# Optimization experiments

Measured on AMD Instinct MI355X. Metric: run time of the kernel, lower is better.

The kernel has to match this reference:

```python
import jax, jax.numpy as jnp
import numpy as np

N_NODES = 100000
N_EDGES = 600000
D = 128
BN_EPS = 1e-5


def setup_inputs() -> dict:
    key = jax.random.key(0)
    k1, k2, k3 = jax.random.split(key, 3)
    x = jax.random.normal(k1, (N_NODES, D), dtype=jnp.float32)
    edge_index = jax.random.randint(k2, (2, N_EDGES), 0, N_NODES, dtype=jnp.int64)
    # Linear(in=D, out=D): kaiming-uniform-ish init
    W = jax.random.normal(k3, (D, D), dtype=jnp.float32) / np.sqrt(D)
    b = jnp.zeros((D,), dtype=jnp.float32)
    eps_gin = jnp.zeros((), dtype=jnp.float32)  # train_eps=True, init 0
    gamma = jnp.ones((D,), dtype=jnp.float32)
    beta = jnp.zeros((D,), dtype=jnp.float32)
    return {"x": x, "edge_index": edge_index, "W": W, "b": b,
            "eps_gin": eps_gin, "gamma": gamma, "beta": beta}


def reference(x, edge_index, W, b, eps_gin, gamma, beta):
    src, dst = edge_index[0], edge_index[1]
    # GIN aggregation: sum of source features into destination nodes
    agg = jax.ops.segment_sum(x[src], dst, num_segments=N_NODES)  # [N, D]
    h = (1.0 + eps_gin) * x + agg
    # MLP([D, D]) == single Linear (PyG plain_last)
    h = jnp.einsum('nd,df->nf', h, W.T) + b  # torch Linear: h @ W^T + b
    # BatchNorm1d in training mode (batch stats, biased variance)
    mean = jnp.mean(h, axis=0)
    var = jnp.mean((h - mean) ** 2, axis=0)
    h = (h - mean) * jax.lax.rsqrt(var + BN_EPS) * gamma + beta
    h = jax.nn.relu(h)
    # residual
    return h + x
```

## Files before the change

### kernel.cpp

```cpp
#include <hip/hip_runtime.h>
#include <hip/hip_bf16.h>
#include <hip/hip_cooperative_groups.h>

namespace cg = cooperative_groups;

#define N_NODES 100000
#define N_EDGES 600000
#define D 128
#define BN_EPS 1e-5f
#define CAP 32
#define CAST_BLOCKS 6250
#define FILL_BLOCKS ((N_EDGES + 255) / 256)

typedef __bf16 bf16x8 __attribute__((ext_vector_type(8)));
typedef float floatx4 __attribute__((ext_vector_type(4)));
typedef unsigned short ushortx8 __attribute__((ext_vector_type(8)));

__device__ __forceinline__ unsigned short f2bf(float f) {
    union { float f; unsigned u; } v; v.f = f;
    unsigned u = v.u;
    unsigned r = u + 0x7FFFu + ((u >> 16) & 1u);
    return (unsigned short)(r >> 16);
}
__device__ __forceinline__ float bf2f(unsigned short u) {
    union { unsigned u; float f; } v; v.u = ((unsigned)u) << 16;
    return v.f;
}

__global__ __launch_bounds__(256) void k_prep(const float* __restrict__ x,
                                              const int* __restrict__ ei,
                                              int* __restrict__ cursor,
                                              int* __restrict__ bucket,
                                              unsigned short* __restrict__ xb) {
    int b = blockIdx.x;
    if (b < CAST_BLOCKS) {
        int idx = (b * 256 + threadIdx.x) * 8;
        float4 a = *(const float4*)(x + idx);
        float4 c = *(const float4*)(x + idx + 4);
        ushortx8 u;
        u[0] = f2bf(a.x); u[1] = f2bf(a.y); u[2] = f2bf(a.z); u[3] = f2bf(a.w);
        u[4] = f2bf(c.x); u[5] = f2bf(c.y); u[6] = f2bf(c.z); u[7] = f2bf(c.w);
        *(ushortx8*)(xb + idx) = u;
    } else {
        int e = (b - CAST_BLOCKS) * 256 + threadIdx.x;
        if (e >= N_EDGES) return;
        int src = ei[e];
        int dst = ei[N_EDGES + e];
        int pos = atomicAdd(&cursor[dst], 1);
        if (pos < CAP) bucket[dst * CAP + pos] = src;
    }
}

__global__ __launch_bounds__(256) void k_aggregate(const unsigned short* __restrict__ xb,
                                                   const int* __restrict__ cursor,
                                                   const int* __restrict__ bucket,
                                                   const float* __restrict__ epsp,
                                                   unsigned short* __restrict__ h) {
    int tid = blockIdx.x * 256 + threadIdx.x;
    int node = tid >> 4;
    if (node >= N_NODES) return;
    int lane = tid & 15;
    int deg = cursor[node];
    if (deg > CAP) deg = CAP;
    const int* bk = bucket + node * CAP;
    float acc[8] = {0.f, 0.f, 0.f, 0.f, 0.f, 0.f, 0.f, 0.f};
    for (int i = 0; i < deg; ++i) {
        int s = bk[i];
        ushortx8 v = *(const ushortx8*)(xb + (size_t)s * D + lane * 8);
#pragma unroll
        for (int j = 0; j < 8; ++j) acc[j] += bf2f(v[j]);
    }
    const float one_eps = 1.0f + epsp[0];
    ushortx8 xv = *(const ushortx8*)(xb + (size_t)node * D + lane * 8);
    ushortx8 o;
#pragma unroll
    for (int j = 0; j < 8; ++j) o[j] = f2bf(one_eps * bf2f(xv[j]) + acc[j]);
    *(ushortx8*)(h + (size_t)node * D + lane * 8) = o;
}

__global__ __launch_bounds__(256) void k_fused(const unsigned short* __restrict__ h,
                                               const float* __restrict__ W,
                                               const float* __restrict__ x,
                                               const float* __restrict__ gamma,
                                               const float* __restrict__ beta,
                                               float* __restrict__ sums,
                                               float* __restrict__ sumsq,
                                               float* __restrict__ out) {
    const int lane = threadIdx.x & 63;
    const int wid  = threadIdx.x >> 6;
    const int gw   = blockIdx.x * 4 + wid;
    const int fhalf = gw & 1;
    const int pair  = gw >> 1;
    const int npairs = gridDim.x * 2;
    const int n16  = lane & 15;
    const int quad = lane >> 4;
    const int fbase = fhalf * 64;

    bf16x8 B[4][4];
#pragma unroll
    for (int ft = 0; ft < 4; ++ft) {
#pragma unroll
        for (int ks = 0; ks < 4; ++ks) {
            const float* wp = W + (fbase + ft * 16 + n16) * D + ks * 32 + quad * 8;
            float4 wa = *(const float4*)wp;
            float4 wb = *(const float4*)(wp + 4);
            ushortx8 u;
            u[0] = f2bf(wa.x); u[1] = f2bf(wa.y); u[2] = f2bf(wa.z); u[3] = f2bf(wa.w);
            u[4] = f2bf(wb.x); u[5] = f2bf(wb.y); u[6] = f2bf(wb.z); u[7] = f2bf(wb.w);
            B[ft][ks] = __builtin_bit_cast(bf16x8, u);
        }
    }

    float psum[4] = {0.f, 0.f, 0.f, 0.f};
    float psq[4]  = {0.f, 0.f, 0.f, 0.f};
    for (int chunk = pair; chunk < N_NODES / 16; chunk += npairs) {
        const int rbase = chunk * 16;
        floatx4 acc[4];
#pragma unroll
        for (int ft = 0; ft < 4; ++ft) acc[ft] = (floatx4){0.f, 0.f, 0.f, 0.f};
#pragma unroll
        for (int ks = 0; ks < 4; ++ks) {
            const unsigned short* hp = h + (size_t)(rbase + n16) * D + ks * 32 + quad * 8;
            bf16x8 a = __builtin_bit_cast(bf16x8, *(const ushortx8*)hp);
#pragma unroll
            for (int ft = 0; ft < 4; ++ft)
                acc[ft] = __builtin_amdgcn_mfma_f32_16x16x32_bf16(a, B[ft][ks], acc[ft], 0, 0, 0);
        }
#pragma unroll
        for (int ft = 0; ft < 4; ++ft) {
#pragma unroll
            for (int i = 0; i < 4; ++i) {
                float v = acc[ft][i];
                psum[ft] += v;
                psq[ft]  += v * v;
            }
        }
    }
#pragma unroll
    for (int ft = 0; ft < 4; ++ft) {
        float s = psum[ft], q = psq[ft];
        s += __shfl_xor(s, 16, 64); q += __shfl_xor(q, 16, 64);
        s += __shfl_xor(s, 32, 64); q += __shfl_xor(q, 32, 64);
        if (quad == 0) {
            atomicAdd(&sums[fbase + ft * 16 + n16], s);
            atomicAdd(&sumsq[fbase + ft * 16 + n16], q);
        }
    }

    cg::this_grid().sync();

    const float inv_n = 1.0f / (float)N_NODES;
    float sc[4], sh[4];
#pragma unroll
    for (int ft = 0; ft < 4; ++ft) {
        int col = fbase + ft * 16 + n16;
        float s = __hip_atomic_load(&sums[col], __ATOMIC_RELAXED, __HIP_MEMORY_SCOPE_AGENT);
        float q = __hip_atomic_load(&sumsq[col], __ATOMIC_RELAXED, __HIP_MEMORY_SCOPE_AGENT);
        float mean = s * inv_n;
        float var  = q * inv_n - mean * mean;
        sc[ft] = gamma[col] * rsqrtf(var + BN_EPS);
        sh[ft] = beta[col] - mean * sc[ft];
    }

    for (int chunk = pair; chunk < N_NODES / 16; chunk += npairs) {
        const int rbase = chunk * 16;
        floatx4 acc[4];
#pragma unroll
        for (int ft = 0; ft < 4; ++ft) acc[ft] = (floatx4){0.f, 0.f, 0.f, 0.f};
#pragma unroll
        for (int ks = 0; ks < 4; ++ks) {
            const unsigned short* hp = h + (size_t)(rbase + n16) * D + ks * 32 + quad * 8;
            bf16x8 a = __builtin_bit_cast(bf16x8, *(const ushortx8*)hp);
#pragma unroll
            for (int ft = 0; ft < 4; ++ft)
                acc[ft] = __builtin_amdgcn_mfma_f32_16x16x32_bf16(a, B[ft][ks], acc[ft], 0, 0, 0);
        }
#pragma unroll
        for (int ft = 0; ft < 4; ++ft) {
            const int col = fbase + ft * 16 + n16;
#pragma unroll
            for (int i = 0; i < 4; ++i) {
                size_t off = (size_t)(rbase + quad * 4 + i) * D + col;
                float v = fmaxf(acc[ft][i] * sc[ft] + sh[ft], 0.0f) + x[off];
                out[off] = v;
            }
        }
    }
}

extern "C" void kernel_launch(void* const* d_in, const int* in_sizes, int n_in,
                              void* d_out, int out_size, void* d_ws, size_t ws_size,
                              hipStream_t stream) {
    const float* x     = (const float*)d_in[0];
    const int*   ei    = (const int*)d_in[1];
    const float* W     = (const float*)d_in[2];
    const float* epsp  = (const float*)d_in[4];
    const float* gamma = (const float*)d_in[5];
    const float* beta  = (const float*)d_in[6];
    float* out = (float*)d_out;

    char* ws = (char*)d_ws;
    int*   cursor = (int*)ws;
    float* sums   = (float*)(ws + (size_t)N_NODES * 4);
    float* sumsq  = sums + D;
    int*   bucket = (int*)(ws + (size_t)N_NODES * 4 + 2 * D * 4);
    unsigned short* xb = (unsigned short*)((char*)bucket + (size_t)N_NODES * CAP * 4);
    unsigned short* h  = xb + (size_t)N_NODES * D;

    hipMemsetAsync(cursor, 0, (size_t)N_NODES * 4 + 2 * D * 4, stream);

    k_prep<<<CAST_BLOCKS + FILL_BLOCKS, 256, 0, stream>>>(x, ei, cursor, bucket, xb);
    k_aggregate<<<(N_NODES * 16 + 255) / 256, 256, 0, stream>>>(xb, cursor, bucket, epsp, h);

    void* args[] = {(void*)&h, (void*)&W, (void*)&x, (void*)&gamma, (void*)&beta,
                    (void*)&sums, (void*)&sumsq, (void*)&out};
    hipLaunchCooperativeKernel((void*)k_fused, dim3(256), dim3(256), args, 0, stream);
}
```

Measured before the change: 257.8 us.

## Split cooperative fused kernel into two launches with a larger grid

Replaces the cooperative kernel and its grid-wide sync with two ordinary kernels: one computes the GEMM and accumulates the BatchNorm statistics, the other recomputes the GEMM and applies normalisation, ReLU and the residual. Dropping the cooperative launch lets the grid grow from 256 to 1024 blocks, which raises occupancy across the many CUs. In exchange there is an extra kernel launch, the W fragments are loaded twice, and the statistics loads become plain reads.

```diff
diff --git a/kernel.cpp b/kernel.cpp
--- a/kernel.cpp
+++ b/kernel.cpp
@@ -1,8 +1,5 @@
 #include <hip/hip_runtime.h>
 #include <hip/hip_bf16.h>
-#include <hip/hip_cooperative_groups.h>
-
-namespace cg = cooperative_groups;
 
 #define N_NODES 100000
 #define N_EDGES 600000
@@ -11,6 +8,7 @@
 #define CAP 32
 #define CAST_BLOCKS 6250
 #define FILL_BLOCKS ((N_EDGES + 255) / 256)
+#define GEMM_GRID 1024
 
 typedef __bf16 bf16x8 __attribute__((ext_vector_type(8)));
 typedef float floatx4 __attribute__((ext_vector_type(4)));
@@ -78,25 +76,9 @@
     *(ushortx8*)(h + (size_t)node * D + lane * 8) = o;
 }
 
-__global__ __launch_bounds__(256) void k_fused(const unsigned short* __restrict__ h,
-                                               const float* __restrict__ W,
-                                               const float* __restrict__ x,
-                                               const float* __restrict__ gamma,
-                                               const float* __restrict__ beta,
-                                               float* __restrict__ sums,
-                                               float* __restrict__ sumsq,
-                                               float* __restrict__ out) {
-    const int lane = threadIdx.x & 63;
-    const int wid  = threadIdx.x >> 6;
-    const int gw   = blockIdx.x * 4 + wid;
-    const int fhalf = gw & 1;
-    const int pair  = gw >> 1;
-    const int npairs = gridDim.x * 2;
-    const int n16  = lane & 15;
-    const int quad = lane >> 4;
-    const int fbase = fhalf * 64;
-
-    bf16x8 B[4][4];
+__device__ __forceinline__ void load_B_frags(const float* __restrict__ W,
+                                             int fbase, int n16, int quad,
+                                             bf16x8 B[4][4]) {
 #pragma unroll
     for (int ft = 0; ft < 4; ++ft) {
 #pragma unroll
@@ -110,6 +92,24 @@
             B[ft][ks] = __builtin_bit_cast(bf16x8, u);
         }
     }
+}
+
+__global__ __launch_bounds__(256) void k_gemm_stats(const unsigned short* __restrict__ h,
+                                                    const float* __restrict__ W,
+                                                    float* __restrict__ sums,
+                                                    float* __restrict__ sumsq) {
+    const int lane = threadIdx.x & 63;
+    const int wid  = threadIdx.x >> 6;
+    const int gw   = blockIdx.x * 4 + wid;
+    const int fhalf = gw & 1;
+    const int pair  = gw >> 1;
+    const int npairs = GEMM_GRID * 2;
+    const int n16  = lane & 15;
+    const int quad = lane >> 4;
+    const int fbase = fhalf * 64;
+
+    bf16x8 B[4][4];
+    load_B_frags(W, fbase, n16, quad, B);
 
     float psum[4] = {0.f, 0.f, 0.f, 0.f};
     float psq[4]  = {0.f, 0.f, 0.f, 0.f};
@@ -146,16 +146,36 @@
             atomicAdd(&sumsq[fbase + ft * 16 + n16], q);
         }
     }
-
-    cg::this_grid().sync();
+}
+
+__global__ __launch_bounds__(256) void k_fin(const unsigned short* __restrict__ h,
+                                             const float* __restrict__ W,
+                                             const float* __restrict__ x,
+                                             const float* __restrict__ sums,
+                                             const float* __restrict__ sumsq,
+                                             const float* __restrict__ gamma,
+                                             const float* __restrict__ beta,
+                                             float* __restrict__ out) {
+    const int lane = threadIdx.x & 63;
+    const int wid  = threadIdx.x >> 6;
+    const int gw   = blockIdx.x * 4 + wid;
+    const int fhalf = gw & 1;
+    const int pair  = gw >> 1;
+    const int npairs = GEMM_GRID * 2;
+    const int n16  = lane & 15;
+    const int quad = lane >> 4;
+    const int fbase = fhalf * 64;
+
+    bf16x8 B[4][4];
+    load_B_frags(W, fbase, n16, quad, B);
 
     const float inv_n = 1.0f / (float)N_NODES;
     float sc[4], sh[4];
 #pragma unroll
     for (int ft = 0; ft < 4; ++ft) {
         int col = fbase + ft * 16 + n16;
-        float s = __hip_atomic_load(&sums[col], __ATOMIC_RELAXED, __HIP_MEMORY_SCOPE_AGENT);
-        float q = __hip_atomic_load(&sumsq[col], __ATOMIC_RELAXED, __HIP_MEMORY_SCOPE_AGENT);
+        float s = sums[col];
+        float q = sumsq[col];
         float mean = s * inv_n;
         float var  = q * inv_n - mean * mean;
         sc[ft] = gamma[col] * rsqrtf(var + BN_EPS);
@@ -181,8 +201,7 @@
 #pragma unroll
             for (int i = 0; i < 4; ++i) {
                 size_t off = (size_t)(rbase + quad * 4 + i) * D + col;
-                float v = fmaxf(acc[ft][i] * sc[ft] + sh[ft], 0.0f) + x[off];
-                out[off] = v;
+                out[off] = fmaxf(acc[ft][i] * sc[ft] + sh[ft], 0.0f) + x[off];
             }
         }
     }
@@ -211,8 +230,6 @@
 
     k_prep<<<CAST_BLOCKS + FILL_BLOCKS, 256, 0, stream>>>(x, ei, cursor, bucket, xb);
     k_aggregate<<<(N_NODES * 16 + 255) / 256, 256, 0, stream>>>(xb, cursor, bucket, epsp, h);
-
-    void* args[] = {(void*)&h, (void*)&W, (void*)&x, (void*)&gamma, (void*)&beta,
-                    (void*)&sums, (void*)&sumsq, (void*)&out};
-    hipLaunchCooperativeKernel((void*)k_fused, dim3(256), dim3(256), args, 0, stream);
-}
+    k_gemm_stats<<<GEMM_GRID, 256, 0, stream>>>(h, W, sums, sumsq);
+    k_fin<<<GEMM_GRID, 256, 0, stream>>>(h, W, x, sums, sumsq, gamma, beta, out);
+}
```

New measurement: 280.4 us. +8.8%, slower.
